# Performance work log

Hardware: AMD Instinct MI355X
Metric: run time of the kernel (lower is better)

The kernel has to match this reference:

```python
import jax, jax.numpy as jnp
import numpy as np

HIDDEN = 2048
N_HEADS = 32
N_KV_HEADS = 8
HEAD_DIM = HIDDEN // N_HEADS  # 64
GROUPS = N_HEADS // N_KV_HEADS  # 4
ROPE_BASE = 10000.0


def _rope_cos_sin(seq_len, dim, dtype):
    inv_freq = 1.0 / (ROPE_BASE ** (jnp.arange(0, dim, 2, dtype=jnp.float32) / dim))
    t = jnp.arange(seq_len, dtype=jnp.float32)
    freqs = jnp.outer(t, inv_freq)            # [S, dim/2]
    emb = jnp.concatenate([freqs, freqs], -1)  # [S, dim]
    return jnp.cos(emb).astype(dtype), jnp.sin(emb).astype(dtype)


def _rotate_half(x):
    x1, x2 = jnp.split(x, 2, axis=-1)
    return jnp.concatenate([-x2, x1], axis=-1)


def setup_inputs() -> dict:
    key = jax.random.key(0)
    ks = jax.random.split(key, 5)
    x = jax.random.normal(ks[0], (2, 2048, HIDDEN), dtype=jnp.float32)
    scale = 0.02
    wq = jax.random.normal(ks[1], (HIDDEN, N_HEADS * HEAD_DIM), dtype=jnp.float32) * scale
    wk = jax.random.normal(ks[2], (HIDDEN, N_KV_HEADS * HEAD_DIM), dtype=jnp.float32) * scale
    wv = jax.random.normal(ks[3], (HIDDEN, N_KV_HEADS * HEAD_DIM), dtype=jnp.float32) * scale
    wo = jax.random.normal(ks[4], (N_HEADS * HEAD_DIM, HIDDEN), dtype=jnp.float32) * scale
    return {"x": x, "wq": wq, "wk": wk, "wv": wv, "wo": wo}


def reference(x, wq, wk, wv, wo):
    b, s, _ = x.shape
    # projections (torch Linear with weight stored transposed -> plain matmul here)
    q = (x @ wq).reshape(b, s, N_HEADS, HEAD_DIM).transpose(0, 2, 1, 3)      # [b,nh,s,d]
    k = (x @ wk).reshape(b, s, N_KV_HEADS, HEAD_DIM).transpose(0, 2, 1, 3)   # [b,kvh,s,d]
    v = (x @ wv).reshape(b, s, N_KV_HEADS, HEAD_DIM).transpose(0, 2, 1, 3)   # [b,kvh,s,d]

    cos, sin = _rope_cos_sin(s, HEAD_DIM, x.dtype)  # [s,d]
    cos = cos[None, None]  # [1,1,s,d]
    sin = sin[None, None]
    q = q * cos + _rotate_half(q) * sin
    k = k * cos + _rotate_half(k) * sin

    # GQA: group query heads per KV head instead of expanding K/V
    qg = q.reshape(b, N_KV_HEADS, GROUPS, s, HEAD_DIM)
    scores = jnp.einsum('bhgqd,bhkd->bhgqk', qg, k) / np.sqrt(HEAD_DIM).astype(x.dtype)
    probs = jax.nn.softmax(scores.astype(jnp.float32), axis=-1).astype(x.dtype)
    out = jnp.einsum('bhgqk,bhkd->bhgqd', probs, v)          # [b,kvh,g,s,d]
    out = out.reshape(b, N_HEADS, s, HEAD_DIM).transpose(0, 2, 1, 3).reshape(b, s, HIDDEN)
    return out @ wo
```

## Files before the change

### kernel.cpp

```cpp
#include <hip/hip_runtime.h>


typedef __bf16 bf16;
typedef __bf16 bf16x4_t __attribute__((ext_vector_type(4)));
typedef __bf16 bf16x8_t __attribute__((ext_vector_type(8)));
typedef float  f32x4_t  __attribute__((ext_vector_type(4)));

#define S_LEN 2048
#define HID   2048
#define NH    32
#define KVH   8
#define HD    64

__device__ __forceinline__ void async_copy16(const void* g, void* l) {
  __builtin_amdgcn_global_load_lds(
      (const __attribute__((address_space(1))) void*)g,
      (__attribute__((address_space(3))) void*)l, 16, 0, 0);
}

__global__ __launch_bounds__(256) void cast_bf16_kernel(
    const float* __restrict__ src, bf16* __restrict__ dst) {
  int i = (blockIdx.x * 256 + threadIdx.x) * 4;
  float4 v = *(const float4*)(src + i);
  bf16x4_t o;
  o[0] = (bf16)v.x; o[1] = (bf16)v.y; o[2] = (bf16)v.z; o[3] = (bf16)v.w;
  *(bf16x4_t*)(dst + i) = o;
}

__global__ __launch_bounds__(256) void wtrans_kernel(
    const float* __restrict__ src, bf16* __restrict__ dst, int C, int dstStride) {
  __shared__ float tile[32][33];
  int c0 = blockIdx.x * 32, r0 = blockIdx.y * 32;
  int t = threadIdx.x;
  int r = t >> 3, c4 = (t & 7) * 4;
  float4 v = *(const float4*)(src + (size_t)(r0 + r) * C + c0 + c4);
  tile[r][c4] = v.x; tile[r][c4 + 1] = v.y; tile[r][c4 + 2] = v.z; tile[r][c4 + 3] = v.w;
  __syncthreads();
  int cc = t >> 3, r4 = (t & 7) * 4;
  bf16x4_t o;
  o[0] = (bf16)tile[r4][cc];     o[1] = (bf16)tile[r4 + 1][cc];
  o[2] = (bf16)tile[r4 + 2][cc]; o[3] = (bf16)tile[r4 + 3][cc];
  *(bf16x4_t*)(dst + (size_t)(c0 + cc) * dstStride + r0 + r4) = o;
}

__global__ __launch_bounds__(256, 2) void qkv_gemm_rope(
    const bf16* __restrict__ A, const bf16* __restrict__ Bt,
    bf16* __restrict__ q_r, bf16* __restrict__ k_r, bf16* __restrict__ v_t) {
  __shared__ char smem[32768];
  char* As = smem;
  char* Bs = smem + 16384;
  const int tid  = threadIdx.x;
  const int wid  = tid >> 6;
  const int lane = tid & 63;
  const int l15  = lane & 15;
  const int quad = lane >> 4;
  const int wm = wid >> 1, wn = wid & 1;
  const int bm = blockIdx.y * 128;
  const int bn = blockIdx.x * 128;
  const int K = 2048;

  f32x4_t acc[4][4] = {};

  for (int k0 = 0; k0 < K; k0 += 64) {
#pragma unroll
    for (int it = 0; it < 4; ++it) {
      int p = it * 256 + tid;
      int row = p >> 3;
      int j = (p & 7) ^ (row & 7);
      async_copy16(A + (size_t)(bm + row) * K + k0 + j * 8,
                   As + (size_t)(it * 256 + wid * 64) * 16);
      async_copy16(Bt + (size_t)(bn + row) * K + k0 + j * 8,
                   Bs + (size_t)(it * 256 + wid * 64) * 16);
    }
    __syncthreads();
#pragma unroll
    for (int kk = 0; kk < 64; kk += 32) {
      bf16x8_t af[4], bfr[4];
      int cbase = (kk >> 3) + quad;
#pragma unroll
      for (int mt = 0; mt < 4; ++mt) {
        int row = wm * 64 + mt * 16 + l15;
        af[mt] = *(const bf16x8_t*)(As + (size_t)(row * 8 + (cbase ^ (row & 7))) * 16);
      }
#pragma unroll
      for (int nt = 0; nt < 4; ++nt) {
        int row = wn * 64 + nt * 16 + l15;
        bfr[nt] = *(const bf16x8_t*)(Bs + (size_t)(row * 8 + (cbase ^ (row & 7))) * 16);
      }
#pragma unroll
      for (int mt = 0; mt < 4; ++mt)
#pragma unroll
        for (int nt = 0; nt < 4; ++nt)
          acc[mt][nt] = __builtin_amdgcn_mfma_f32_16x16x32_bf16(
              af[mt], bfr[nt], acc[mt][nt], 0, 0, 0);
    }
    __syncthreads();
  }

  const int cb = blockIdx.x * 2 + wn;
  const int rowbase = bm + wm * 64;
  const int bidx = bm >> 11;
  const float LE = 0.41524101186098285f;
  const float SC = 0.18033688011112043f;

  if (cb < 40) {
    const bool isQ = (cb < 32);
    const float sc = isQ ? SC : 1.0f;
    bf16* base = isQ ? (q_r + (size_t)(bidx * NH + cb) * S_LEN * HD)
                     : (k_r + (size_t)(bidx * KVH + (cb - 32)) * S_LEN * HD);
#pragma unroll
    for (int nt = 0; nt < 2; ++nt) {
      int i = nt * 16 + l15;
      float inv = __builtin_exp2f(-(float)i * LE);
#pragma unroll
      for (int mt = 0; mt < 4; ++mt)
#pragma unroll
        for (int r = 0; r < 4; ++r) {
          int row = rowbase + mt * 16 + quad * 4 + r;
          int s = row & 2047;
          float ang = (float)s * inv;
          float sv, cv;
          __sincosf(ang, &sv, &cv);
          float x1 = acc[mt][nt][r], x2 = acc[mt][nt + 2][r];
          bf16* d = base + (size_t)s * HD;
          d[i]      = (bf16)((x1 * cv - x2 * sv) * sc);
          d[i + 32] = (bf16)((x2 * cv + x1 * sv) * sc);
        }
    }
  } else {
    const int kvh = cb - 40;
    bf16* base = v_t + (size_t)(bidx * KVH + kvh) * HD * S_LEN;
#pragma unroll
    for (int nt = 0; nt < 4; ++nt) {
      int d = nt * 16 + l15;
#pragma unroll
      for (int mt = 0; mt < 4; ++mt) {
        int s0 = (rowbase + mt * 16 + quad * 4) & 2047;
        bf16x4_t o;
        o[0] = (bf16)acc[mt][nt][0]; o[1] = (bf16)acc[mt][nt][1];
        o[2] = (bf16)acc[mt][nt][2]; o[3] = (bf16)acc[mt][nt][3];
        *(bf16x4_t*)(base + (size_t)d * S_LEN + s0) = o;
      }
    }
  }
}

template <typename OutT>
__global__ __launch_bounds__(256, 2) void gemm_bt(
    const bf16* __restrict__ A, const bf16* __restrict__ Bt,
    OutT* __restrict__ C, int N, int K) {
  __shared__ char smem[32768];
  char* As = smem;
  char* Bs = smem + 16384;
  const int tid  = threadIdx.x;
  const int wid  = tid >> 6;
  const int lane = tid & 63;
  const int l15  = lane & 15;
  const int quad = lane >> 4;
  const int wm = wid >> 1, wn = wid & 1;
  const int bm = blockIdx.y * 128;
  const int bn = blockIdx.x * 128;

  f32x4_t acc[4][4] = {};

  for (int k0 = 0; k0 < K; k0 += 64) {
#pragma unroll
    for (int it = 0; it < 4; ++it) {
      int p = it * 256 + tid;
      int row = p >> 3;
      int j = (p & 7) ^ (row & 7);
      async_copy16(A + (size_t)(bm + row) * K + k0 + j * 8,
                   As + (size_t)(it * 256 + wid * 64) * 16);
      async_copy16(Bt + (size_t)(bn + row) * K + k0 + j * 8,
                   Bs + (size_t)(it * 256 + wid * 64) * 16);
    }
    __syncthreads();
#pragma unroll
    for (int kk = 0; kk < 64; kk += 32) {
      bf16x8_t af[4], bfr[4];
      int cbase = (kk >> 3) + quad;
#pragma unroll
      for (int mt = 0; mt < 4; ++mt) {
        int row = wm * 64 + mt * 16 + l15;
        af[mt] = *(const bf16x8_t*)(As + (size_t)(row * 8 + (cbase ^ (row & 7))) * 16);
      }
#pragma unroll
      for (int nt = 0; nt < 4; ++nt) {
        int row = wn * 64 + nt * 16 + l15;
        bfr[nt] = *(const bf16x8_t*)(Bs + (size_t)(row * 8 + (cbase ^ (row & 7))) * 16);
      }
#pragma unroll
      for (int mt = 0; mt < 4; ++mt)
#pragma unroll
        for (int nt = 0; nt < 4; ++nt)
          acc[mt][nt] = __builtin_amdgcn_mfma_f32_16x16x32_bf16(
              af[mt], bfr[nt], acc[mt][nt], 0, 0, 0);
    }
    __syncthreads();
  }
#pragma unroll
  for (int mt = 0; mt < 4; ++mt)
#pragma unroll
    for (int nt = 0; nt < 4; ++nt)
#pragma unroll
      for (int r = 0; r < 4; ++r) {
        int row = bm + wm * 64 + mt * 16 + quad * 4 + r;
        int col = bn + wn * 64 + nt * 16 + l15;
        C[(size_t)row * N + col] = (OutT)acc[mt][nt][r];
      }
}

__global__ __launch_bounds__(256, 3) void attn_kernel(
    const bf16* __restrict__ q_r, const bf16* __restrict__ k_r,
    const bf16* __restrict__ v_t, bf16* __restrict__ attn) {
  __shared__ char smem[49152];
  char* Ks = smem;
  char* Vs = smem + 16384;
  char* Ps = smem + 32768;
  const int tid = threadIdx.x;
  const int wid = tid >> 6;
  const int lane = tid & 63;
  const int l15 = lane & 15, quad = lane >> 4;
  const int qh = quad >> 1, ql = quad & 1;
  const int blky = blockIdx.y;
  const int b = blky >> 3, kvh = blky & 7;
  const int h = kvh * 4 + wid;
  const int q0 = blockIdx.x * 32;
  char* Pw = Ps + wid * 4096;

  const bf16* Kg = k_r + (size_t)blky * S_LEN * HD;
  const bf16* Vg = v_t + (size_t)blky * HD * S_LEN;

  bf16x8_t qf0[2], qf1[2];
#pragma unroll
  for (int qt = 0; qt < 2; ++qt) {
    const bf16* qb = q_r + ((size_t)(b * NH + h) * S_LEN + q0 + qt * 16 + l15) * HD;
    qf0[qt] = *(const bf16x8_t*)(qb + quad * 8);
    qf1[qt] = *(const bf16x8_t*)(qb + 32 + quad * 8);
  }
  bf16x8_t ones;
#pragma unroll
  for (int e = 0; e < 8; ++e) ones[e] = (bf16)1.0f;

  f32x4_t o_acc[2][4] = {};
  f32x4_t l_acc[2] = {};

#pragma unroll
  for (int it = 0; it < 4; ++it) {
    int p = it * 256 + tid;
    int row = p >> 3, j = (p & 7) ^ (row & 7);
    async_copy16(Kg + (size_t)row * HD + j * 8,
                 Ks + (size_t)(it * 256 + wid * 64) * 16);
  }

  for (int kt = 0; kt < S_LEN / 128; ++kt) {
    __syncthreads();
#pragma unroll
    for (int it = 0; it < 4; ++it) {
      int p = it * 256 + tid;
      int vrow = p >> 4, vj = (p & 15) ^ (vrow & 15);
      async_copy16(Vg + (size_t)vrow * S_LEN + kt * 128 + vj * 8,
                   Vs + (size_t)(it * 256 + wid * 64) * 16);
    }

    f32x4_t sa[2][8];
#pragma unroll
    for (int t = 0; t < 8; ++t) { sa[0][t] = f32x4_t{0.f,0.f,0.f,0.f}; sa[1][t] = f32x4_t{0.f,0.f,0.f,0.f}; }
#pragma unroll
    for (int t = 0; t < 8; ++t) {
      int row = t * 16 + l15;
      int s3 = l15 & 7;
      bf16x8_t kf0 = *(const bf16x8_t*)(Ks + (size_t)(row * 8 + (quad ^ s3)) * 16);
      bf16x8_t kf1 = *(const bf16x8_t*)(Ks + (size_t)(row * 8 + ((4 + quad) ^ s3)) * 16);
      sa[0][t] = __builtin_amdgcn_mfma_f32_16x16x32_bf16(kf0, qf0[0], sa[0][t], 0, 0, 0);
      sa[0][t] = __builtin_amdgcn_mfma_f32_16x16x32_bf16(kf1, qf1[0], sa[0][t], 0, 0, 0);
      sa[1][t] = __builtin_amdgcn_mfma_f32_16x16x32_bf16(kf0, qf0[1], sa[1][t], 0, 0, 0);
      sa[1][t] = __builtin_amdgcn_mfma_f32_16x16x32_bf16(kf1, qf1[1], sa[1][t], 0, 0, 0);
    }
    __syncthreads();

    if (kt < S_LEN / 128 - 1) {
#pragma unroll
      for (int it = 0; it < 4; ++it) {
        int p = it * 256 + tid;
        int row = p >> 3, j = (p & 7) ^ (row & 7);
        async_copy16(Kg + (size_t)((kt + 1) * 128 + row) * HD + j * 8,
                     Ks + (size_t)(it * 256 + wid * 64) * 16);
      }
    }

#pragma unroll
    for (int qt = 0; qt < 2; ++qt) {
#pragma unroll
      for (int t = 0; t < 8; ++t) {
        bf16x4_t pk;
        pk[0] = (bf16)__builtin_exp2f(sa[qt][t][0]);
        pk[1] = (bf16)__builtin_exp2f(sa[qt][t][1]);
        pk[2] = (bf16)__builtin_exp2f(sa[qt][t][2]);
        pk[3] = (bf16)__builtin_exp2f(sa[qt][t][3]);
        *(bf16x4_t*)(Pw + l15 * 256 + (((2 * t + qh) ^ l15) * 16) + ql * 8) = pk;
      }
#pragma unroll
      for (int c = 0; c < 4; ++c) {
        bf16x8_t pf = *(const bf16x8_t*)(Pw + l15 * 256 + (((4 * c + quad) ^ l15) * 16));
        l_acc[qt] = __builtin_amdgcn_mfma_f32_16x16x32_bf16(ones, pf, l_acc[qt], 0, 0, 0);
#pragma unroll
        for (int nt = 0; nt < 4; ++nt) {
          int d = nt * 16 + l15;
          bf16x8_t vf = *(const bf16x8_t*)(Vs + d * 256 + (((4 * c + quad) ^ l15) * 16));
          o_acc[qt][nt] = __builtin_amdgcn_mfma_f32_16x16x32_bf16(vf, pf, o_acc[qt][nt], 0, 0, 0);
        }
      }
    }
  }

#pragma unroll
  for (int qt = 0; qt < 2; ++qt) {
    float inv = 1.0f / l_acc[qt][0];
#pragma unroll
    for (int nt = 0; nt < 4; ++nt) {
      bf16x4_t o;
      o[0] = (bf16)(o_acc[qt][nt][0] * inv);
      o[1] = (bf16)(o_acc[qt][nt][1] * inv);
      o[2] = (bf16)(o_acc[qt][nt][2] * inv);
      o[3] = (bf16)(o_acc[qt][nt][3] * inv);
      *(bf16x4_t*)(Pw + l15 * 144 + (nt * 16 + quad * 4) * 2) = o;
    }
    int row = lane >> 2, cc = lane & 3;
    bf16x8_t r0 = *(const bf16x8_t*)(Pw + row * 144 + cc * 32);
    bf16x8_t r1 = *(const bf16x8_t*)(Pw + row * 144 + cc * 32 + 16);
    int token = q0 + qt * 16 + row;
    bf16* dst = attn + ((size_t)(b * S_LEN + token)) * HID + h * 64 + cc * 16;
    *(bf16x8_t*)dst = r0;
    *(bf16x8_t*)(dst + 8) = r1;
  }
}

extern "C" void kernel_launch(void* const* d_in, const int* in_sizes, int n_in,
                              void* d_out, int out_size, void* d_ws, size_t ws_size,
                              hipStream_t stream) {
  const float* x  = (const float*)d_in[0];
  const float* wq = (const float*)d_in[1];
  const float* wk = (const float*)d_in[2];
  const float* wv = (const float*)d_in[3];
  const float* wo = (const float*)d_in[4];
  float* out = (float*)d_out;
  char* ws = (char*)d_ws;

  bf16* q_r    = (bf16*)(ws + 0);
  bf16* k_r    = (bf16*)(ws + 16777216);
  bf16* v_t    = (bf16*)(ws + 20971520);
  bf16* wqkv_t = (bf16*)(ws + 25165824);
  bf16* attn   = (bf16*)(ws + 25165824);
  bf16* wo_t   = (bf16*)(ws + 16777216);
  bf16* x_b    = (bf16*)d_out;

  cast_bf16_kernel<<<8192, 256, 0, stream>>>(x, x_b);
  wtrans_kernel<<<dim3(64, 64), 256, 0, stream>>>(wq, wqkv_t, 2048, 2048);
  wtrans_kernel<<<dim3(16, 64), 256, 0, stream>>>(wk, wqkv_t + (size_t)2048 * 2048, 512, 2048);
  wtrans_kernel<<<dim3(16, 64), 256, 0, stream>>>(wv, wqkv_t + (size_t)2560 * 2048, 512, 2048);

  qkv_gemm_rope<<<dim3(24, 32), 256, 0, stream>>>(x_b, wqkv_t, q_r, k_r, v_t);
  attn_kernel<<<dim3(64, 16), 256, 0, stream>>>(q_r, k_r, v_t, attn);

  wtrans_kernel<<<dim3(64, 64), 256, 0, stream>>>(wo, wo_t, 2048, 2048);
  gemm_bt<float><<<dim3(16, 32), 256, 0, stream>>>(attn, wo_t, out, 2048, 2048);
}
```

Before: 358.6 us.

## Keep softmax probabilities in registers via permlane swap, skipping LDS round trip

The attention kernel no longer writes exp'd scores to shared memory and reads them back as MFMA operands. It packs them with v_cvt_pk_bf16_f32 and rearranges lanes with v_permlane32_swap, and compensates by permuting the K row order during the global-to-LDS load so the score layout matches the PV operand layout. This removes the per-tile P buffer traffic and cuts shared memory from 48KB to 32KB, which may allow more resident blocks. It relies on the row permutation and lane-swap mapping being exactly right, and it raises register pressure by holding pf in registers across the barrier.

```diff
diff --git a/kernel.cpp b/kernel.cpp
--- a/kernel.cpp
+++ b/kernel.cpp
@@ -5,6 +5,8 @@
 typedef __bf16 bf16x4_t __attribute__((ext_vector_type(4)));
 typedef __bf16 bf16x8_t __attribute__((ext_vector_type(8)));
 typedef float  f32x4_t  __attribute__((ext_vector_type(4)));
+typedef unsigned int u32;
+typedef unsigned int u32x4_t __attribute__((ext_vector_type(4)));
 
 #define S_LEN 2048
 #define HID   2048
@@ -16,6 +18,16 @@
   __builtin_amdgcn_global_load_lds(
       (const __attribute__((address_space(1))) void*)g,
       (__attribute__((address_space(3))) void*)l, 16, 0, 0);
+}
+
+__device__ __forceinline__ u32 cvt_pk_bf16(float lo, float hi) {
+  u32 r;
+  asm("v_cvt_pk_bf16_f32 %0, %1, %2" : "=v"(r) : "v"(lo), "v"(hi));
+  return r;
+}
+
+__device__ __forceinline__ void permlane32_swap(u32& a, u32& b) {
+  asm("v_permlane32_swap_b32 %0, %1" : "+v"(a), "+v"(b));
 }
 
 __global__ __launch_bounds__(256) void cast_bf16_kernel(
@@ -213,20 +225,17 @@
 __global__ __launch_bounds__(256, 3) void attn_kernel(
     const bf16* __restrict__ q_r, const bf16* __restrict__ k_r,
     const bf16* __restrict__ v_t, bf16* __restrict__ attn) {
-  __shared__ char smem[49152];
+  __shared__ char smem[32768];
   char* Ks = smem;
   char* Vs = smem + 16384;
-  char* Ps = smem + 32768;
   const int tid = threadIdx.x;
   const int wid = tid >> 6;
   const int lane = tid & 63;
   const int l15 = lane & 15, quad = lane >> 4;
-  const int qh = quad >> 1, ql = quad & 1;
   const int blky = blockIdx.y;
   const int b = blky >> 3, kvh = blky & 7;
   const int h = kvh * 4 + wid;
   const int q0 = blockIdx.x * 32;
-  char* Pw = Ps + wid * 4096;
 
   const bf16* Kg = k_r + (size_t)blky * S_LEN * HD;
   const bf16* Vg = v_t + (size_t)blky * HD * S_LEN;
@@ -249,7 +258,8 @@
   for (int it = 0; it < 4; ++it) {
     int p = it * 256 + tid;
     int row = p >> 3, j = (p & 7) ^ (row & 7);
-    async_copy16(Kg + (size_t)row * HD + j * 8,
+    int gr = (row & ~12) | ((row & 4) << 1) | ((row & 8) >> 1);
+    async_copy16(Kg + (size_t)gr * HD + j * 8,
                  Ks + (size_t)(it * 256 + wid * 64) * 16);
   }
 
@@ -277,6 +287,27 @@
       sa[1][t] = __builtin_amdgcn_mfma_f32_16x16x32_bf16(kf0, qf0[1], sa[1][t], 0, 0, 0);
       sa[1][t] = __builtin_amdgcn_mfma_f32_16x16x32_bf16(kf1, qf1[1], sa[1][t], 0, 0, 0);
     }
+
+    bf16x8_t pf[2][4];
+#pragma unroll
+    for (int qt = 0; qt < 2; ++qt)
+#pragma unroll
+      for (int c = 0; c < 4; ++c) {
+        u32 w0 = cvt_pk_bf16(__builtin_exp2f(sa[qt][2 * c][0]),
+                             __builtin_exp2f(sa[qt][2 * c][1]));
+        u32 w1 = cvt_pk_bf16(__builtin_exp2f(sa[qt][2 * c][2]),
+                             __builtin_exp2f(sa[qt][2 * c][3]));
+        u32 w2 = cvt_pk_bf16(__builtin_exp2f(sa[qt][2 * c + 1][0]),
+                             __builtin_exp2f(sa[qt][2 * c + 1][1]));
+        u32 w3 = cvt_pk_bf16(__builtin_exp2f(sa[qt][2 * c + 1][2]),
+                             __builtin_exp2f(sa[qt][2 * c + 1][3]));
+        permlane32_swap(w0, w2);
+        permlane32_swap(w1, w3);
+        u32x4_t pw;
+        pw[0] = w0; pw[1] = w1; pw[2] = w2; pw[3] = w3;
+        pf[qt][c] = __builtin_bit_cast(bf16x8_t, pw);
+      }
+
     __syncthreads();
 
     if (kt < S_LEN / 128 - 1) {
@@ -284,36 +315,27 @@
       for (int it = 0; it < 4; ++it) {
         int p = it * 256 + tid;
         int row = p >> 3, j = (p & 7) ^ (row & 7);
-        async_copy16(Kg + (size_t)((kt + 1) * 128 + row) * HD + j * 8,
+        int gr = (row & ~12) | ((row & 4) << 1) | ((row & 8) >> 1);
+        async_copy16(Kg + (size_t)((kt + 1) * 128 + gr) * HD + j * 8,
                      Ks + (size_t)(it * 256 + wid * 64) * 16);
       }
     }
 
 #pragma unroll
-    for (int qt = 0; qt < 2; ++qt) {
-#pragma unroll
-      for (int t = 0; t < 8; ++t) {
-        bf16x4_t pk;
-        pk[0] = (bf16)__builtin_exp2f(sa[qt][t][0]);
-        pk[1] = (bf16)__builtin_exp2f(sa[qt][t][1]);
-        pk[2] = (bf16)__builtin_exp2f(sa[qt][t][2]);
-        pk[3] = (bf16)__builtin_exp2f(sa[qt][t][3]);
-        *(bf16x4_t*)(Pw + l15 * 256 + (((2 * t + qh) ^ l15) * 16) + ql * 8) = pk;
-      }
+    for (int qt = 0; qt < 2; ++qt)
 #pragma unroll
       for (int c = 0; c < 4; ++c) {
-        bf16x8_t pf = *(const bf16x8_t*)(Pw + l15 * 256 + (((4 * c + quad) ^ l15) * 16));
-        l_acc[qt] = __builtin_amdgcn_mfma_f32_16x16x32_bf16(ones, pf, l_acc[qt], 0, 0, 0);
+        l_acc[qt] = __builtin_amdgcn_mfma_f32_16x16x32_bf16(ones, pf[qt][c], l_acc[qt], 0, 0, 0);
 #pragma unroll
         for (int nt = 0; nt < 4; ++nt) {
           int d = nt * 16 + l15;
           bf16x8_t vf = *(const bf16x8_t*)(Vs + d * 256 + (((4 * c + quad) ^ l15) * 16));
-          o_acc[qt][nt] = __builtin_amdgcn_mfma_f32_16x16x32_bf16(vf, pf, o_acc[qt][nt], 0, 0, 0);
+          o_acc[qt][nt] = __builtin_amdgcn_mfma_f32_16x16x32_bf16(vf, pf[qt][c], o_acc[qt][nt], 0, 0, 0);
         }
       }
-    }
-  }
-
+  }
+
+  char* Pw = smem + wid * 4096;
 #pragma unroll
   for (int qt = 0; qt < 2; ++qt) {
     float inv = 1.0f / l_acc[qt][0];
```

Measured after the change: 353.3 us. Within noise of the previous version (-1.5%).
